# Optimization experiments

Hardware: AMD Instinct MI355X
Metric: run time of the kernel (lower is better)

The kernel has to match this reference:

```python
import jax, jax.numpy as jnp
import numpy as np

N_NODES = 50000
N_EDGES = 800000
D = 256          # in_features == out_features == num_classes
T = 4            # number of replicas / linear heads
NS = 64          # num_edges (hyperedges)


def setup_inputs() -> dict:
    key = jax.random.key(0)
    ks = jax.random.split(key, 10)
    s = D ** -0.5
    return {
        "edge_index": jax.random.randint(ks[0], (2, N_EDGES), 0, N_NODES, dtype=jnp.int64)
        if jax.config.jax_enable_x64 else jax.random.randint(ks[0], (2, N_EDGES), 0, N_NODES, dtype=jnp.int32),
        "features": jax.random.normal(ks[1], (N_NODES, D), jnp.float32),
        "lin_w": jax.random.normal(ks[2], (T, D, D), jnp.float32) * s,
        "lin_b": jax.random.normal(ks[3], (T, D), jnp.float32) * 0.01,
        "gcn0_w": jax.random.normal(ks[4], (D, D), jnp.float32) * s,
        "gcn0_b": jax.random.normal(ks[5], (D,), jnp.float32) * 0.01,
        "gcn1_w": jax.random.normal(ks[6], (D, D), jnp.float32) * s,
        "gcn1_b": jax.random.normal(ks[7], (D,), jnp.float32) * 0.01,
        "lin1_w": jax.random.normal(ks[8], (D, NS), jnp.float32) * s,
        "lin1_b": jax.random.normal(ks[9], (NS,), jnp.float32) * 0.01,
    }


def _l2_normalize(x, eps=1e-8):
    n = jnp.sqrt(jnp.sum(x * x, axis=-1, keepdims=True))
    return x / jnp.maximum(n, eps)


def reference(edge_index, features, lin_w, lin_b, gcn0_w, gcn0_b, gcn1_w, gcn1_b, lin1_w, lin1_b):
    num_nodes, d = features.shape
    t = lin_w.shape[0]
    ns = lin1_w.shape[1]
    scale = d ** -0.5  # out_features ** -0.5

    # t linear projections: (t, N, D)
    transformed = jnp.einsum('nd,tdk->tnk', features, lin_w) + lin_b[:, None, :]

    src, dst = edge_index[0], edge_index[1]
    # cosine similarity of features[src] vs each replica's transformed[dst]
    fs = _l2_normalize(features)[src]              # (E, D)
    tf_n = _l2_normalize(transformed)              # (t, N, D)
    sim = jnp.stack([jnp.sum(fs * tf_n[i][dst], axis=-1) for i in range(t)], axis=1)  # (E, t)
    best_idx = jnp.argmax(sim, axis=1)
    best_dst = dst + best_idx.astype(dst.dtype) * num_nodes

    # extra per-replica identity edges: node n -> node n + i*N, i in [0, t)
    ar = jnp.arange(num_nodes, dtype=src.dtype)
    extra_src = jnp.tile(ar, t)
    extra_dst = (ar[None, :] + (jnp.arange(t, dtype=src.dtype) * num_nodes)[:, None]).reshape(-1)

    src_all = jnp.concatenate([src, src, extra_src])
    dst_all = jnp.concatenate([dst, best_dst, extra_dst])
    n_total = (t + 1) * num_nodes

    # PyG gcn_norm: drop pre-existing self loops (weight 0), add one self loop per node,
    # symmetric normalization with degree from destination index.
    loops = jnp.arange(n_total, dtype=src.dtype)
    src2 = jnp.concatenate([src_all, loops])
    dst2 = jnp.concatenate([dst_all, loops])
    w2 = jnp.concatenate([jnp.where(src_all == dst_all, 0.0, 1.0).astype(features.dtype),
                          jnp.ones(n_total, features.dtype)])
    deg = jax.ops.segment_sum(w2, dst2, num_segments=n_total)
    dinv = jnp.where(deg > 0, jax.lax.rsqrt(deg), 0.0)
    norm = w2 * dinv[src2] * dinv[dst2]

    def gcn(x, W, b):
        xw = x @ W
        return jax.ops.segment_sum(norm[:, None] * xw[src2], dst2, num_segments=n_total) + b

    all_features = jnp.concatenate([features, transformed.reshape(t * num_nodes, d)], axis=0)
    # dropout is identity in eval mode
    h = jax.nn.relu(all_features)
    h = gcn(h, gcn0_w, gcn0_b)
    h = jax.nn.relu(h)
    all_features2 = gcn(h, gcn1_w, gcn1_b)          # ((t+1)N, D)
    logits = jax.nn.relu(all_features2) @ lin1_w + lin1_b  # ((t+1)N, NS)

    # H[n, c] counts how many of the (t+1) replicas assign node n to cluster c
    classes = jnp.argmax(logits.reshape(t + 1, num_nodes, ns), axis=-1)  # (t+1, N)
    H = jax.nn.one_hot(classes, ns, dtype=features.dtype).sum(axis=0)     # (N, NS)

    # hyperedge features: sum of all_features2 over base-replica nodes in each hyperedge
    mask = (H > 0).astype(features.dtype)                                  # (N, NS)
    hyperedge_features = mask.T @ all_features2[:num_nodes]                # (NS, D)

    dots = (all_features @ hyperedge_features.T) * scale                   # ((t+1)N, NS)
    return H, hyperedge_features, dots
```

## Files before the change

### kernel.cpp

```cpp
#include <hip/hip_runtime.h>

#define D 256
#define T 4
#define NS 64

typedef unsigned int uint32;
typedef short s16x8 __attribute__((ext_vector_type(8)));
typedef float f32x4 __attribute__((ext_vector_type(4)));

__device__ __forceinline__ float bflo(uint32 u) { return __uint_as_float(u << 16); }
__device__ __forceinline__ float bfhi(uint32 u) { return __uint_as_float(u & 0xffff0000u); }
__device__ __forceinline__ unsigned short f2bf(float x) {
    uint32 u = __float_as_uint(x);
    u = u + 0x7FFFu + ((u >> 16) & 1u);
    return (unsigned short)(u >> 16);
}
__device__ __forceinline__ uint32 pack2(float a, float b) {
    return (uint32)f2bf(a) | ((uint32)f2bf(b) << 16);
}
__device__ __forceinline__ uint32 relu2(uint32 u) {
    uint32 s = u & 0x80008000u;
    uint32 m = ((s >> 15) ^ 0x00010001u) * 0xFFFFu;
    return u & m;
}

__global__ void zero_kernel(uint32* __restrict__ p, long long n)
{
    long long i = (long long)blockIdx.x * blockDim.x + threadIdx.x;
    long long st = (long long)gridDim.x * blockDim.x;
    for (; i < n; i += st) p[i] = 0u;
}

__global__ void f2bf_kernel(const float* __restrict__ in, unsigned short* __restrict__ out,
                            long long n8)
{
    long long i = (long long)blockIdx.x * blockDim.x + threadIdx.x;
    long long st = (long long)gridDim.x * blockDim.x;
    for (; i < n8; i += st) {
        float4 a = *(const float4*)(in + i * 8);
        float4 b = *(const float4*)(in + i * 8 + 4);
        uint4 o;
        o.x = pack2(a.x, a.y); o.y = pack2(a.z, a.w);
        o.z = pack2(b.x, b.y); o.w = pack2(b.z, b.w);
        *(uint4*)(out + i * 8) = o;
    }
}

__global__ void wfrag_kernel(const float* __restrict__ g0, const float* __restrict__ g1,
                             const float* __restrict__ lw, unsigned short* __restrict__ out)
{
    int o = blockIdx.x * 256 + threadIdx.x;
    int mat = blockIdx.y;
    const float* W = (mat == 0) ? g0 : (mat == 1) ? g1 : (lw + (size_t)(mat - 2) * 65536);
    int j = o & 7, lane = (o >> 3) & 63, ks = (o >> 9) & 7, nt = o >> 12;
    int n15 = lane & 15, quad = lane >> 4;
    int k = ks * 32 + quad * 8 + j;
    int n = nt * 16 + n15;
    out[(size_t)mat * 65536 + o] = f2bf(W[(size_t)k * 256 + n]);
}

__global__ __launch_bounds__(256, 2)
void gemm_mfma(const unsigned short* __restrict__ A,
               const unsigned short* __restrict__ Wfrag,
               const float* __restrict__ bias,
               unsigned short* __restrict__ Cout,
               int M, int nStripes)
{
    __shared__ unsigned short Asm[64 * 264];
    int t = threadIdx.x, w = t >> 6, lane = t & 63;
    int n15 = lane & 15, quad = lane >> 4;
    int z = blockIdx.y;
    Wfrag += (size_t)z * 65536;
    bias  += (size_t)z * 256;
    Cout  += (size_t)z * (size_t)M * 256;

    s16x8 bfr[4][8];
#pragma unroll
    for (int nt = 0; nt < 4; nt++)
#pragma unroll
        for (int ks = 0; ks < 8; ks++)
            bfr[nt][ks] = *(const s16x8*)(Wfrag +
                (size_t)(((w * 4 + nt) * 8 + ks) * 64 + lane) * 8);

    float bcol[4];
#pragma unroll
    for (int nt = 0; nt < 4; nt++) bcol[nt] = bias[(w * 4 + nt) * 16 + n15];

    for (int s = blockIdx.x; s < nStripes; s += gridDim.x) {
        int m0 = s * 64;
        __syncthreads();
#pragma unroll
        for (int i = 0; i < 8; i++) {
            int idx = i * 256 + t;
            int m = idx >> 5, kc = (idx & 31) * 8;
            int gm = m0 + m;
            uint4 v = make_uint4(0u, 0u, 0u, 0u);
            if (gm < M) v = *(const uint4*)(A + (size_t)gm * 256 + kc);
            *(uint4*)(Asm + m * 264 + kc) = v;
        }
        __syncthreads();

        f32x4 acc[4][4];
#pragma unroll
        for (int rt = 0; rt < 4; rt++)
#pragma unroll
            for (int nt = 0; nt < 4; nt++)
#pragma unroll
                for (int e = 0; e < 4; e++) acc[rt][nt][e] = 0.f;

#pragma unroll
        for (int rt = 0; rt < 4; rt++) {
            int abase = (rt * 16 + n15) * 264 + quad * 8;
#pragma unroll
            for (int ks = 0; ks < 8; ks++) {
                s16x8 a = *(const s16x8*)(Asm + abase + ks * 32);
#pragma unroll
                for (int nt = 0; nt < 4; nt++)
                    acc[rt][nt] = __builtin_amdgcn_mfma_f32_16x16x32_bf16(
                        a, bfr[nt][ks], acc[rt][nt], 0, 0, 0);
            }
        }

#pragma unroll
        for (int rt = 0; rt < 4; rt++) {
            int row0 = m0 + rt * 16 + quad * 4;
#pragma unroll
            for (int nt = 0; nt < 4; nt++) {
                int colp = (w * 4 + nt) * 16 + n15;
#pragma unroll
                for (int r = 0; r < 4; r++) {
                    int gr = row0 + r;
                    if (gr < M)
                        Cout[(size_t)gr * 256 + colp] = f2bf(acc[rt][nt][r] + bcol[nt]);
                }
            }
        }
    }
}

__global__ __launch_bounds__(256)
void tinv_kernel(const unsigned short* __restrict__ tr, float* __restrict__ tinv, int rows)
{
    int wave = threadIdx.x >> 6, lane = threadIdx.x & 63;
    int r = blockIdx.x * 4 + wave;
    if (r >= rows) return;
    uint2 q = *(const uint2*)(tr + (size_t)r * D + lane * 4);
    float a = bflo(q.x), b = bfhi(q.x), c = bflo(q.y), d = bfhi(q.y);
    float s = a * a + b * b + c * c + d * d;
#pragma unroll
    for (int off = 32; off; off >>= 1) s += __shfl_xor(s, off);
    if (lane == 0) tinv[r] = 1.f / fmaxf(sqrtf(s), 1e-8f);
}

__global__ void ehist_kernel(const int* __restrict__ dst, int* __restrict__ ecnt, int E)
{
    for (int e = blockIdx.x * blockDim.x + threadIdx.x; e < E;
         e += gridDim.x * blockDim.x)
        atomicAdd(ecnt + dst[e], 1);
}

__global__ void escatter_kernel(const int* __restrict__ src, const int* __restrict__ dst,
                                const int* __restrict__ eptr, int* __restrict__ efill,
                                uint2* __restrict__ esorted, int E)
{
    for (int e = blockIdx.x * blockDim.x + threadIdx.x; e < E;
         e += gridDim.x * blockDim.x) {
        int d = dst[e];
        int pos = eptr[d] + atomicAdd(efill + d, 1);
        esorted[pos] = make_uint2((uint32)src[e], (uint32)d);
    }
}

__global__ __launch_bounds__(256)
void sim3_kernel(const uint2* __restrict__ esorted,
                 const unsigned short* __restrict__ featb,
                 const unsigned short* __restrict__ tr, const float* __restrict__ tinv,
                 int* __restrict__ bestS, int E, int Nn)
{
    int w = threadIdx.x >> 6, lane = threadIdx.x & 63;
    int n15 = lane & 15, quad = lane >> 4;
    int base = (blockIdx.x * 4 + w) * 16;
    if (base >= E) return;
    int ei = min(base + n15, E - 1);
    uint2 se = esorted[ei];
    const unsigned short* arow = featb + (size_t)se.x * D + quad * 8;
    const unsigned short* brow = tr + (size_t)se.y * D + quad * 8;
    size_t rstride = (size_t)Nn * D;

    f32x4 a0 = {0.f, 0.f, 0.f, 0.f}, a1 = a0, a2 = a0, a3 = a0;
#pragma unroll
    for (int ks = 0; ks < 8; ks++) {
        s16x8 a  = *(const s16x8*)(arow + ks * 32);
        s16x8 b0 = *(const s16x8*)(brow + ks * 32);
        s16x8 b1 = *(const s16x8*)(brow + rstride + ks * 32);
        s16x8 b2 = *(const s16x8*)(brow + 2 * rstride + ks * 32);
        s16x8 b3 = *(const s16x8*)(brow + 3 * rstride + ks * 32);
        a0 = __builtin_amdgcn_mfma_f32_16x16x32_bf16(a, b0, a0, 0, 0, 0);
        a1 = __builtin_amdgcn_mfma_f32_16x16x32_bf16(a, b1, a1, 0, 0, 0);
        a2 = __builtin_amdgcn_mfma_f32_16x16x32_bf16(a, b2, a2, 0, 0, 0);
        a3 = __builtin_amdgcn_mfma_f32_16x16x32_bf16(a, b3, a3, 0, 0, 0);
    }
    if (quad == (n15 >> 2) && base + n15 < E) {
        int r = n15 & 3;
        int d = (int)se.y;
        float v0 = a0[r] * tinv[d];
        float v1 = a1[r] * tinv[Nn + d];
        float v2 = a2[r] * tinv[2 * Nn + d];
        float v3 = a3[r] * tinv[3 * Nn + d];
        float bv = v0; int bi = 0;
        if (v1 > bv) { bv = v1; bi = 1; }
        if (v2 > bv) { bv = v2; bi = 2; }
        if (v3 > bv) { bv = v3; bi = 3; }
        bestS[base + n15] = bi;
    }
}

__device__ __forceinline__ void decode_edge(int e, const uint2* __restrict__ esorted,
                                            const int* __restrict__ bestS,
                                            int E, int Nn, int& s, int& d, bool& keep)
{
    if (e < E) {
        uint2 se = esorted[e];
        s = (int)se.x; d = (int)se.y; keep = (s != d);
    } else if (e < 2 * E) {
        int k = e - E;
        uint2 se = esorted[k];
        s = (int)se.x; d = (int)se.y + bestS[k] * Nn; keep = (s != d);
    } else if (e < 2 * E + T * Nn) {
        int k = e - 2 * E; int i = k / Nn; int n = k - i * Nn;
        s = n; d = n + i * Nn; keep = (i != 0);
    } else {
        int v = e - (2 * E + T * Nn); s = v; d = v; keep = true;
    }
}

__global__ void hist_kernel(const uint2* __restrict__ esorted, const int* __restrict__ bestS,
                            int* __restrict__ cnt, int E, int Nn)
{
    int total = 2 * E + (2 * T + 1) * Nn;
    for (int e = blockIdx.x * blockDim.x + threadIdx.x; e < total;
         e += gridDim.x * blockDim.x) {
        int s, d; bool keep;
        decode_edge(e, esorted, bestS, E, Nn, s, d, keep);
        if (keep) atomicAdd(cnt + d, 1);
    }
}

__global__ void dinv_kernel(const int* __restrict__ cnt, float* __restrict__ dinv, int n)
{
    int v = blockIdx.x * blockDim.x + threadIdx.x;
    if (v < n) dinv[v] = (cnt[v] > 0) ? rsqrtf((float)cnt[v]) : 0.f;
}

__global__ void emeta_kernel(const uint2* __restrict__ esorted, const int* __restrict__ bestS,
                             const float* __restrict__ dinv, uint2* __restrict__ emeta, int E)
{
    for (int e = blockIdx.x * blockDim.x + threadIdx.x; e < E;
         e += gridDim.x * blockDim.x) {
        uint2 se = esorted[e];
        uint32 packed = se.x | ((uint32)bestS[e] << 27);
        emeta[e] = make_uint2(packed, __float_as_uint(dinv[se.x]));
    }
}

__global__ void scan_sums(const int* __restrict__ cnt, int* __restrict__ aux, int n)
{
    __shared__ int sd[256];
    int idx = blockIdx.x * 256 + threadIdx.x;
    sd[threadIdx.x] = (idx < n) ? cnt[idx] : 0;
    __syncthreads();
    for (int off = 128; off; off >>= 1) {
        if (threadIdx.x < off) sd[threadIdx.x] += sd[threadIdx.x + off];
        __syncthreads();
    }
    if (threadIdx.x == 0) aux[blockIdx.x] = sd[0];
}

__global__ void scan_aux(const int* __restrict__ aux, int* __restrict__ auxex, int nb)
{
    __shared__ int sd[1024];
    int t = threadIdx.x;
    int v = (t < nb) ? aux[t] : 0;
    sd[t] = v;
    __syncthreads();
    for (int off = 1; off < 1024; off <<= 1) {
        int x = (t >= off) ? sd[t - off] : 0;
        __syncthreads();
        sd[t] += x;
        __syncthreads();
    }
    if (t < nb) auxex[t] = sd[t] - v;
}

__global__ void scan_write(const int* __restrict__ cnt, const int* __restrict__ auxex,
                           int* __restrict__ rowptr, int n)
{
    __shared__ int sd[256];
    int t = threadIdx.x;
    int idx = blockIdx.x * 256 + t;
    int v = (idx < n) ? cnt[idx] : 0;
    sd[t] = v;
    __syncthreads();
    for (int off = 1; off < 256; off <<= 1) {
        int x = (t >= off) ? sd[t - off] : 0;
        __syncthreads();
        sd[t] += x;
        __syncthreads();
    }
    if (idx < n) {
        int rp = auxex[blockIdx.x] + sd[t] - v;
        rowptr[idx] = rp;
        if (idx == n - 1) rowptr[n] = rp + v;
    }
}

__global__ __launch_bounds__(256)
void agg5_kernel(const int* __restrict__ eptr, const uint2* __restrict__ emeta,
                 const unsigned short* __restrict__ xa,
                 const unsigned short* __restrict__ xb,
                 const float* __restrict__ dinv,
                 unsigned short* __restrict__ outb, int Nn)
{
    int wave = threadIdx.x >> 6, lane = threadIdx.x & 63;
    int v = blockIdx.x * 4 + wave;
    if (v >= Nn) return;

    float dv  = dinv[v];
    float dr1 = dinv[v + Nn];
    float dr2 = dinv[v + 2 * Nn];
    float dr3 = dinv[v + 3 * Nn];
    float dr4 = dinv[v + 4 * Nn];

    uint2 qv = *(const uint2*)(xa + (size_t)v * D + lane * 4);
    qv.x = relu2(qv.x); qv.y = relu2(qv.y);
    float y0 = bflo(qv.x), y1 = bfhi(qv.x), y2 = bflo(qv.y), y3 = bfhi(qv.y);

    float wsb = dv * dv;
    float b0 = wsb * y0, b1 = wsb * y1, b2 = wsb * y2, b3 = wsb * y3;

    float wi1 = dv * dr1, wi2 = dv * dr2, wi3 = dv * dr3;
    float r10 = wi1 * y0, r11 = wi1 * y1, r12 = wi1 * y2, r13 = wi1 * y3;
    float r20 = wi2 * y0, r21 = wi2 * y1, r22 = wi2 * y2, r23 = wi2 * y3;
    float r30 = wi3 * y0, r31 = wi3 * y1, r32 = wi3 * y2, r33 = wi3 * y3;
    float r40 = 0.f, r41 = 0.f, r42 = 0.f, r43 = 0.f;

    {
        uint2 q = *(const uint2*)(xb + ((size_t)0 * Nn + v) * D + lane * 4);
        q.x = relu2(q.x); q.y = relu2(q.y);
        float ws = dr1 * dr1;
        r10 = fmaf(ws, bflo(q.x), r10); r11 = fmaf(ws, bfhi(q.x), r11);
        r12 = fmaf(ws, bflo(q.y), r12); r13 = fmaf(ws, bfhi(q.y), r13);
    }
    {
        uint2 q = *(const uint2*)(xb + ((size_t)1 * Nn + v) * D + lane * 4);
        q.x = relu2(q.x); q.y = relu2(q.y);
        float ws = dr2 * dr2;
        r20 = fmaf(ws, bflo(q.x), r20); r21 = fmaf(ws, bfhi(q.x), r21);
        r22 = fmaf(ws, bflo(q.y), r22); r23 = fmaf(ws, bfhi(q.y), r23);
    }
    {
        uint2 q = *(const uint2*)(xb + ((size_t)2 * Nn + v) * D + lane * 4);
        q.x = relu2(q.x); q.y = relu2(q.y);
        float ws = dr3 * dr3;
        r30 = fmaf(ws, bflo(q.x), r30); r31 = fmaf(ws, bfhi(q.x), r31);
        r32 = fmaf(ws, bflo(q.y), r32); r33 = fmaf(ws, bfhi(q.y), r33);
    }
    {
        uint2 q = *(const uint2*)(xb + ((size_t)3 * Nn + v) * D + lane * 4);
        q.x = relu2(q.x); q.y = relu2(q.y);
        float ws = dr4 * dr4;
        r40 = fmaf(ws, bflo(q.x), r40); r41 = fmaf(ws, bfhi(q.x), r41);
        r42 = fmaf(ws, bflo(q.y), r42); r43 = fmaf(ws, bfhi(q.y), r43);
    }

    int j = eptr[v], jend = eptr[v + 1];

#define EDGE_BODY(qq, ss, bb, ww)                                                  \
    {                                                                              \
        float x0 = bflo(qq.x), x1 = bfhi(qq.x), x2 = bflo(qq.y), x3 = bfhi(qq.y);  \
        float wb = (ss != v) ? (ww) * dv : 0.f;                                    \
        if (bb == 0) wb += wb;                                                     \
        b0 = fmaf(wb, x0, b0); b1 = fmaf(wb, x1, b1);                              \
        b2 = fmaf(wb, x2, b2); b3 = fmaf(wb, x3, b3);                              \
        if (bb == 1) {                                                             \
            float wr = (ww) * dr1;                                                 \
            r10 = fmaf(wr, x0, r10); r11 = fmaf(wr, x1, r11);                      \
            r12 = fmaf(wr, x2, r12); r13 = fmaf(wr, x3, r13);                      \
        } else if (bb == 2) {                                                      \
            float wr = (ww) * dr2;                                                 \
            r20 = fmaf(wr, x0, r20); r21 = fmaf(wr, x1, r21);                      \
            r22 = fmaf(wr, x2, r22); r23 = fmaf(wr, x3, r23);                      \
        } else if (bb == 3) {                                                      \
            float wr = (ww) * dr3;                                                 \
            r30 = fmaf(wr, x0, r30); r31 = fmaf(wr, x1, r31);                      \
            r32 = fmaf(wr, x2, r32); r33 = fmaf(wr, x3, r33);                      \
        }                                                                          \
    }

    for (; j + 2 <= jend; j += 2) {
        uint2 m0 = emeta[j];
        uint2 m1 = emeta[j + 1];
        uint32 su0 = (uint32)__builtin_amdgcn_readfirstlane((int)m0.x);
        uint32 su1 = (uint32)__builtin_amdgcn_readfirstlane((int)m1.x);
        float ws0 = __uint_as_float((uint32)__builtin_amdgcn_readfirstlane((int)m0.y));
        float ws1 = __uint_as_float((uint32)__builtin_amdgcn_readfirstlane((int)m1.y));
        int s0 = (int)(su0 & 0x07FFFFFFu), bx0 = (int)(su0 >> 27);
        int s1 = (int)(su1 & 0x07FFFFFFu), bx1 = (int)(su1 >> 27);
        uint2 q0 = *(const uint2*)(xa + (size_t)s0 * D + lane * 4);
        uint2 q1 = *(const uint2*)(xa + (size_t)s1 * D + lane * 4);
        q0.x = relu2(q0.x); q0.y = relu2(q0.y);
        q1.x = relu2(q1.x); q1.y = relu2(q1.y);
        EDGE_BODY(q0, s0, bx0, ws0);
        EDGE_BODY(q1, s1, bx1, ws1);
    }
    if (j < jend) {
        uint2 m0 = emeta[j];
        uint32 su0 = (uint32)__builtin_amdgcn_readfirstlane((int)m0.x);
        float ws0 = __uint_as_float((uint32)__builtin_amdgcn_readfirstlane((int)m0.y));
        int s0 = (int)(su0 & 0x07FFFFFFu), bx0 = (int)(su0 >> 27);
        uint2 q0 = *(const uint2*)(xa + (size_t)s0 * D + lane * 4);
        q0.x = relu2(q0.x); q0.y = relu2(q0.y);
        EDGE_BODY(q0, s0, bx0, ws0);
    }
#undef EDGE_BODY

    uint2 o;
    o.x = pack2(b0, b1); o.y = pack2(b2, b3);
    *(uint2*)(outb + (size_t)v * D + lane * 4) = o;
    o.x = pack2(r10, r11); o.y = pack2(r12, r13);
    *(uint2*)(outb + ((size_t)v + Nn) * D + lane * 4) = o;
    o.x = pack2(r20, r21); o.y = pack2(r22, r23);
    *(uint2*)(outb + ((size_t)v + 2 * (size_t)Nn) * D + lane * 4) = o;
    o.x = pack2(r30, r31); o.y = pack2(r32, r33);
    *(uint2*)(outb + ((size_t)v + 3 * (size_t)Nn) * D + lane * 4) = o;
    o.x = pack2(r40, r41); o.y = pack2(r42, r43);
    *(uint2*)(outb + ((size_t)v + 4 * (size_t)Nn) * D + lane * 4) = o;
}

__global__ __launch_bounds__(256, 2)
void logits_mfma(const unsigned short* __restrict__ af2, const float* __restrict__ Wl,
                 const float* __restrict__ bl, float* __restrict__ H,
                 int M, int Nn, int nStripes)
{
    __shared__ unsigned short Asm[64 * 264];
    int t = threadIdx.x, w = t >> 6, lane = t & 63;
    int n15 = lane & 15, quad = lane >> 4;

    s16x8 bfr[4][8];
#pragma unroll
    for (int nt = 0; nt < 4; nt++)
#pragma unroll
        for (int ks = 0; ks < 8; ks++) {
            s16x8 f;
#pragma unroll
            for (int j = 0; j < 8; j++) {
                int k = ks * 32 + quad * 8 + j;
                f[j] = (short)f2bf(Wl[(size_t)k * NS + nt * 16 + n15]);
            }
            bfr[nt][ks] = f;
        }
    float bcol[4];
#pragma unroll
    for (int nt = 0; nt < 4; nt++) bcol[nt] = bl[nt * 16 + n15];

    for (int s = blockIdx.x; s < nStripes; s += gridDim.x) {
        int m0 = s * 64;
        __syncthreads();
#pragma unroll
        for (int i = 0; i < 8; i++) {
            int idx = i * 256 + t;
            int m = idx >> 5, kc = (idx & 31) * 8;
            int gm = m0 + m;
            uint4 v = make_uint4(0u, 0u, 0u, 0u);
            if (gm < M) {
                v = *(const uint4*)(af2 + (size_t)gm * 256 + kc);
                v.x = relu2(v.x); v.y = relu2(v.y);
                v.z = relu2(v.z); v.w = relu2(v.w);
            }
            *(uint4*)(Asm + m * 264 + kc) = v;
        }
        __syncthreads();

        f32x4 acc[4];
#pragma unroll
        for (int nt = 0; nt < 4; nt++)
#pragma unroll
            for (int e = 0; e < 4; e++) acc[nt][e] = 0.f;

        int abase = (w * 16 + n15) * 264 + quad * 8;
#pragma unroll
        for (int ks = 0; ks < 8; ks++) {
            s16x8 a = *(const s16x8*)(Asm + abase + ks * 32);
#pragma unroll
            for (int nt = 0; nt < 4; nt++)
                acc[nt] = __builtin_amdgcn_mfma_f32_16x16x32_bf16(
                    a, bfr[nt][ks], acc[nt], 0, 0, 0);
        }

#pragma unroll
        for (int e = 0; e < 4; e++) {
            float bv = acc[0][e] + bcol[0]; int bi = n15;
#pragma unroll
            for (int nt = 1; nt < 4; nt++) {
                float v = acc[nt][e] + bcol[nt];
                int c = nt * 16 + n15;
                if (v > bv) { bv = v; bi = c; }
            }
#pragma unroll
            for (int off = 1; off < 16; off <<= 1) {
                float ov = __shfl_xor(bv, off);
                int   oi = __shfl_xor(bi, off);
                if (ov > bv || (ov == bv && oi < bi)) { bv = ov; bi = oi; }
            }
            if (n15 == 0) {
                int gr = m0 + w * 16 + quad * 4 + e;
                if (gr < M) atomicAdd(H + (size_t)(gr % Nn) * NS + bi, 1.0f);
            }
        }
    }
}

__global__ __launch_bounds__(64)
void he_kernel(const float* __restrict__ H, const unsigned short* __restrict__ af2,
               float* __restrict__ he, int Nn)
{
    __shared__ float acc[NS * D];
    int lane = threadIdx.x;
    for (int i = lane * 4; i < NS * D; i += 256)
        *(float4*)(acc + i) = make_float4(0.f, 0.f, 0.f, 0.f);
    __syncthreads();
    int n0 = blockIdx.x * 128;
    int n1 = min(n0 + 128, Nn);
    for (int n = n0; n < n1; n++) {
        float hv = H[(size_t)n * NS + lane];
        unsigned long long m = __ballot(hv > 0.f);
        if (!m) continue;
        uint2 q = *(const uint2*)(af2 + (size_t)n * D + lane * 4);
        float x0 = bflo(q.x), x1 = bfhi(q.x), x2 = bflo(q.y), x3 = bfhi(q.y);
        while (m) {
            int c = __ffsll(m) - 1;
            m &= m - 1;
            float* p = acc + (size_t)c * D + lane * 4;
            p[0] += x0; p[1] += x1; p[2] += x2; p[3] += x3;
        }
    }
    __syncthreads();
    for (int i = lane; i < NS * D; i += 64) atomicAdd(he + i, acc[i]);
}

__global__ void bigb_copy(const float* __restrict__ he, float* __restrict__ BigB)
{
    int idx = blockIdx.x * 256 + threadIdx.x;
    if (idx < D * NS) {
        int d = idx >> 6, c = idx & 63;
        BigB[idx] = he[(size_t)c * D + d];
    }
}

__global__ __launch_bounds__(256)
void bigb_mm(const float* __restrict__ lin_w, const float* __restrict__ lin_b,
             const float* __restrict__ he, float* __restrict__ BigB,
             float* __restrict__ beta)
{
    int gw = (int)((blockIdx.x * 256 + threadIdx.x) >> 6);
    int lane = threadIdx.x & 63;
    const int totalA = T * D * NS;
    if (gw >= totalA + T * NS) return;
    const float* xrow; const float* hrow; float* outp;
    if (gw < totalA) {
        int t = gw / (D * NS); int rem = gw - t * D * NS;
        int d = rem / NS; int c = rem - d * NS;
        xrow = lin_w + ((size_t)t * D + d) * D;
        hrow = he + (size_t)c * D;
        outp = BigB + ((size_t)(t + 1) * D + d) * NS + c;
    } else {
        int i = gw - totalA; int t = i / NS; int c = i - t * NS;
        xrow = lin_b + (size_t)t * D;
        hrow = he + (size_t)c * D;
        outp = beta + (size_t)(t + 1) * NS + c;
    }
    float4 x = *(const float4*)(xrow + lane * 4);
    float4 h = *(const float4*)(hrow + lane * 4);
    float s = x.x * h.x + x.y * h.y + x.z * h.z + x.w * h.w;
#pragma unroll
    for (int off = 32; off; off >>= 1) s += __shfl_xor(s, off);
    if (lane == 0) *outp = s;
}

__global__ __launch_bounds__(256, 2)
void dots_mfma(const float* __restrict__ feat, const float* __restrict__ BigB,
               const float* __restrict__ beta, float* __restrict__ dots,
               int Nn, int nStripes)
{
    __shared__ unsigned short Asm[64 * 264];
    int t = threadIdx.x, w = t >> 6, lane = t & 63;
    int n15 = lane & 15, quad = lane >> 4;
    int rho = blockIdx.y;
    const float* Bp = BigB + (size_t)rho * D * NS;

    s16x8 bfr[4][8];
#pragma unroll
    for (int nt = 0; nt < 4; nt++)
#pragma unroll
        for (int ks = 0; ks < 8; ks++) {
            s16x8 f;
#pragma unroll
            for (int j = 0; j < 8; j++) {
                int k = ks * 32 + quad * 8 + j;
                f[j] = (short)f2bf(Bp[(size_t)k * NS + nt * 16 + n15]);
            }
            bfr[nt][ks] = f;
        }
    float bcol[4];
#pragma unroll
    for (int nt = 0; nt < 4; nt++) bcol[nt] = beta[rho * NS + nt * 16 + n15];

    for (int s = blockIdx.x; s < nStripes; s += gridDim.x) {
        int m0 = s * 64;
        __syncthreads();
#pragma unroll
        for (int i = 0; i < 8; i++) {
            int idx = i * 256 + t;
            int m = idx >> 5, kc = (idx & 31) * 8;
            int gm = m0 + m;
            uint4 o = make_uint4(0u, 0u, 0u, 0u);
            if (gm < Nn) {
                float4 a = *(const float4*)(feat + (size_t)gm * 256 + kc);
                float4 b = *(const float4*)(feat + (size_t)gm * 256 + kc + 4);
                o.x = pack2(a.x, a.y); o.y = pack2(a.z, a.w);
                o.z = pack2(b.x, b.y); o.w = pack2(b.z, b.w);
            }
            *(uint4*)(Asm + m * 264 + kc) = o;
        }
        __syncthreads();

        f32x4 acc[4];
#pragma unroll
        for (int nt = 0; nt < 4; nt++)
#pragma unroll
            for (int e = 0; e < 4; e++) acc[nt][e] = 0.f;

        int abase = (w * 16 + n15) * 264 + quad * 8;
#pragma unroll
        for (int ks = 0; ks < 8; ks++) {
            s16x8 a = *(const s16x8*)(Asm + abase + ks * 32);
#pragma unroll
            for (int nt = 0; nt < 4; nt++)
                acc[nt] = __builtin_amdgcn_mfma_f32_16x16x32_bf16(
                    a, bfr[nt][ks], acc[nt], 0, 0, 0);
        }

#pragma unroll
        for (int e = 0; e < 4; e++) {
            int gr = m0 + w * 16 + quad * 4 + e;
            if (gr >= Nn) continue;
#pragma unroll
            for (int nt = 0; nt < 4; nt++) {
                int c = nt * 16 + n15;
                dots[((size_t)rho * Nn + gr) * NS + c] = (acc[nt][e] + bcol[nt]) * 0.0625f;
            }
        }
    }
}

extern "C" void kernel_launch(void* const* d_in, const int* in_sizes, int n_in,
                              void* d_out, int out_size, void* d_ws, size_t ws_size,
                              hipStream_t stream)
{
    const int*   edge_index = (const int*)d_in[0];
    const float* features   = (const float*)d_in[1];
    const float* lin_w      = (const float*)d_in[2];
    const float* lin_b      = (const float*)d_in[3];
    const float* gcn0_w     = (const float*)d_in[4];
    const float* gcn0_b     = (const float*)d_in[5];
    const float* gcn1_w     = (const float*)d_in[6];
    const float* gcn1_b     = (const float*)d_in[7];
    const float* lin1_w     = (const float*)d_in[8];
    const float* lin1_b     = (const float*)d_in[9];

    int E  = in_sizes[0] / 2;
    int Nn = in_sizes[1] / D;
    int n_total = (T + 1) * Nn;
    int Mrep = T * Nn;

    const int* src = edge_index;
    const int* dst = edge_index + E;

    float* out_H    = (float*)d_out;
    float* out_he   = out_H + (size_t)Nn * NS;
    float* out_dots = out_he + (size_t)NS * D;

    char* ws = (char*)d_ws;
    auto carve = [&](size_t bytes) {
        char* p = ws; ws += (bytes + 255) & ~(size_t)255; return p;
    };
    unsigned short* R1   = (unsigned short*)carve((size_t)n_total * D * 2);
    unsigned short* R2   = (unsigned short*)carve((size_t)n_total * D * 2);
    float*          BigB = (float*)carve((size_t)(T + 1) * D * NS * 4);
    float*          beta = (float*)carve((size_t)(T + 1) * NS * 4);
    unsigned short* transformed = R2;

    char* sc = (char*)out_dots;
    auto carve2 = [&](size_t bytes) {
        char* p = sc; sc += (bytes + 255) & ~(size_t)255; return p;
    };
    float* tinv    = (float*)carve2((size_t)Mrep * 4);
    int*   best    = (int*)carve2((size_t)E * 4);
    int*   cnt     = (int*)carve2((size_t)n_total * 4);
    float* dinv    = (float*)carve2((size_t)n_total * 4);
    int*   aux     = (int*)carve2(1024 * 4);
    int*   auxex   = (int*)carve2(1024 * 4);
    unsigned short* featb  = (unsigned short*)carve2((size_t)Nn * D * 2);
    unsigned short* Wfrags = (unsigned short*)carve2((size_t)6 * 65536 * 2);
    int*   ecnt    = (int*)carve2((size_t)Nn * 4);
    int*   eptr    = (int*)carve2((size_t)(Nn + 1) * 4);
    int*   efill   = (int*)carve2((size_t)Nn * 4);
    uint2* esorted = (uint2*)carve2((size_t)E * 8);
    uint2* emeta   = (uint2*)carve2((size_t)E * 8);

    zero_kernel<<<512, 256, 0, stream>>>((uint32*)cnt, n_total);
    zero_kernel<<<512, 256, 0, stream>>>((uint32*)ecnt, Nn);
    zero_kernel<<<512, 256, 0, stream>>>((uint32*)efill, Nn);
    zero_kernel<<<512, 256, 0, stream>>>((uint32*)out_H, (long long)Nn * NS + NS * D);
    zero_kernel<<<1, 256, 0, stream>>>((uint32*)beta, (T + 1) * NS);

    wfrag_kernel<<<dim3(256, 6), 256, 0, stream>>>(gcn0_w, gcn1_w, lin_w, Wfrags);
    f2bf_kernel<<<2048, 256, 0, stream>>>(features, featb, (long long)Nn * D / 8);

    int strN = (Nn + 63) / 64;
    gemm_mfma<<<dim3(512, T), 256, 0, stream>>>(featb, Wfrags + 2 * 65536, lin_b,
                                                transformed, Nn, strN);
    tinv_kernel<<<(Mrep + 3) / 4, 256, 0, stream>>>(transformed, tinv, Mrep);

    ehist_kernel<<<2048, 256, 0, stream>>>(dst, ecnt, E);
    int enb = (Nn + 255) / 256;
    scan_sums<<<enb, 256, 0, stream>>>(ecnt, aux, Nn);
    scan_aux<<<1, 1024, 0, stream>>>(aux, auxex, enb);
    scan_write<<<enb, 256, 0, stream>>>(ecnt, auxex, eptr, Nn);
    escatter_kernel<<<2048, 256, 0, stream>>>(src, dst, eptr, efill, esorted, E);
    int nGroups = (E + 15) / 16;
    sim3_kernel<<<(nGroups + 3) / 4, 256, 0, stream>>>(esorted, featb, transformed,
                                                       tinv, best, E, Nn);

    hist_kernel<<<2048, 256, 0, stream>>>(esorted, best, cnt, E, Nn);
    dinv_kernel<<<(n_total + 255) / 256, 256, 0, stream>>>(cnt, dinv, n_total);
    emeta_kernel<<<2048, 256, 0, stream>>>(esorted, best, dinv, emeta, E);

    int strT = (n_total + 63) / 64;
    agg5_kernel<<<(Nn + 3) / 4, 256, 0, stream>>>(eptr, emeta, featb, transformed,
                                                  dinv, R1, Nn);
    gemm_mfma<<<dim3(512, 1), 256, 0, stream>>>(R1, Wfrags, gcn0_b, R1, n_total, strT);

    agg5_kernel<<<(Nn + 3) / 4, 256, 0, stream>>>(eptr, emeta, R1, R1 + (size_t)Nn * D,
                                                  dinv, R2, Nn);
    gemm_mfma<<<dim3(512, 1), 256, 0, stream>>>(R2, Wfrags + 65536, gcn1_b, R2,
                                                n_total, strT);

    logits_mfma<<<512, 256, 0, stream>>>(R2, lin1_w, lin1_b, out_H, n_total, Nn, strT);

    he_kernel<<<(Nn + 127) / 128, 64, 0, stream>>>(out_H, R2, out_he, Nn);

    bigb_copy<<<(D * NS + 255) / 256, 256, 0, stream>>>(out_he, BigB);
    bigb_mm<<<(T * D * NS + T * NS + 3) / 4, 256, 0, stream>>>(lin_w, lin_b, out_he,
                                                               BigB, beta);
    dots_mfma<<<dim3(160, 5), 256, 0, stream>>>(features, BigB, beta, out_dots,
                                                Nn, strN);
}
```

Measured before the change: 1.072 ms.

## Restructure hyperedge sum via transposed mask and reuse bf16 features in dots

The old hyperedge kernel walked nodes serially per block and accumulated into a 64KB shared buffer, then flushed it with many global atomics. It is replaced by a kernel that writes a transposed byte mask of H, followed by a per-(cluster, node-chunk) warp reduction that gathers the selected af2 rows in registers and issues one atomic per element. Separately, the bf16 feature copy is placed in workspace when space allows so the dots kernel can read bf16 directly instead of converting fp32 again. Work is now proportional to nonzero mask entries, with one gather per entry rather than a shared-memory update, and there is an extra kernel launch plus mask memory traffic.

```diff
diff --git a/kernel.cpp b/kernel.cpp
--- a/kernel.cpp
+++ b/kernel.cpp
@@ -520,32 +520,72 @@
     }
 }
 
-__global__ __launch_bounds__(64)
-void he_kernel(const float* __restrict__ H, const unsigned short* __restrict__ af2,
-               float* __restrict__ he, int Nn)
-{
-    __shared__ float acc[NS * D];
-    int lane = threadIdx.x;
-    for (int i = lane * 4; i < NS * D; i += 256)
-        *(float4*)(acc + i) = make_float4(0.f, 0.f, 0.f, 0.f);
+__global__ __launch_bounds__(256)
+void maskT_kernel(const float* __restrict__ H, unsigned char* __restrict__ maskT, int Nn)
+{
+    __shared__ unsigned char tile[64 * 80];
+    int t = threadIdx.x;
+    int n0 = blockIdx.x * 64;
+    int c = t & 63, rr = t >> 6;
+#pragma unroll
+    for (int i = 0; i < 16; i++) {
+        int n = rr + i * 4;
+        float hv = (n0 + n < Nn) ? H[(size_t)(n0 + n) * NS + c] : 0.f;
+        tile[c * 80 + n] = (hv > 0.f) ? 1 : 0;
+    }
     __syncthreads();
-    int n0 = blockIdx.x * 128;
-    int n1 = min(n0 + 128, Nn);
-    for (int n = n0; n < n1; n++) {
-        float hv = H[(size_t)n * NS + lane];
-        unsigned long long m = __ballot(hv > 0.f);
-        if (!m) continue;
-        uint2 q = *(const uint2*)(af2 + (size_t)n * D + lane * 4);
-        float x0 = bflo(q.x), x1 = bfhi(q.x), x2 = bflo(q.y), x3 = bfhi(q.y);
-        while (m) {
-            int c = __ffsll(m) - 1;
-            m &= m - 1;
-            float* p = acc + (size_t)c * D + lane * 4;
-            p[0] += x0; p[1] += x1; p[2] += x2; p[3] += x3;
-        }
-    }
-    __syncthreads();
-    for (int i = lane; i < NS * D; i += 64) atomicAdd(he + i, acc[i]);
+    int cc = t >> 2, ns = (t & 3) * 16;
+    if (n0 + ns < Nn) {
+        uint4 v = *(const uint4*)(tile + cc * 80 + ns);
+        *(uint4*)(maskT + (size_t)cc * Nn + n0 + ns) = v;
+    }
+}
+
+#define HE_NSPLIT 64
+__global__ __launch_bounds__(256)
+void he2_kernel(const unsigned char* __restrict__ maskT,
+                const unsigned short* __restrict__ af2,
+                float* __restrict__ he, int Nn, int chunk)
+{
+    int w = threadIdx.x >> 6, lane = threadIdx.x & 63;
+    int gw = blockIdx.x * 4 + w;
+    int c = gw / HE_NSPLIT;
+    int s = gw - c * HE_NSPLIT;
+    int n0 = s * chunk;
+    int n1 = min(n0 + chunk, Nn);
+    if (n0 >= n1) return;
+    const unsigned char* mrow = maskT + (size_t)c * Nn;
+    float a0 = 0.f, a1 = 0.f, a2 = 0.f, a3 = 0.f;
+
+    for (int nb = n0; nb < n1; nb += 256) {
+        uint32 mb = 0;
+        if (n1 - nb >= 256) {
+            mb = *(const uint32*)(mrow + nb + lane * 4);
+        } else {
+#pragma unroll
+            for (int k = 0; k < 4; k++) {
+                int n = nb + lane * 4 + k;
+                if (n < n1) mb |= ((uint32)mrow[n]) << (8 * k);
+            }
+        }
+#pragma unroll
+        for (int k = 0; k < 4; k++) {
+            unsigned long long m = __ballot(((mb >> (8 * k)) & 0xffu) != 0u);
+            while (m) {
+                int l = __ffsll(m) - 1;
+                m &= m - 1;
+                int n = nb + l * 4 + k;
+                uint2 q = *(const uint2*)(af2 + (size_t)n * D + lane * 4);
+                a0 += bflo(q.x); a1 += bfhi(q.x);
+                a2 += bflo(q.y); a3 += bfhi(q.y);
+            }
+        }
+    }
+    float* p = he + (size_t)c * D + lane * 4;
+    atomicAdd(p + 0, a0);
+    atomicAdd(p + 1, a1);
+    atomicAdd(p + 2, a2);
+    atomicAdd(p + 3, a3);
 }
 
 __global__ void bigb_copy(const float* __restrict__ he, float* __restrict__ BigB)
@@ -588,7 +628,9 @@
 }
 
 __global__ __launch_bounds__(256, 2)
-void dots_mfma(const float* __restrict__ feat, const float* __restrict__ BigB,
+void dots_mfma(const unsigned short* __restrict__ featb,
+               const float* __restrict__ feat32, int useBf,
+               const float* __restrict__ BigB,
                const float* __restrict__ beta, float* __restrict__ dots,
                int Nn, int nStripes)
 {
@@ -625,10 +667,14 @@
             int gm = m0 + m;
             uint4 o = make_uint4(0u, 0u, 0u, 0u);
             if (gm < Nn) {
-                float4 a = *(const float4*)(feat + (size_t)gm * 256 + kc);
-                float4 b = *(const float4*)(feat + (size_t)gm * 256 + kc + 4);
-                o.x = pack2(a.x, a.y); o.y = pack2(a.z, a.w);
-                o.z = pack2(b.x, b.y); o.w = pack2(b.z, b.w);
+                if (useBf) {
+                    o = *(const uint4*)(featb + (size_t)gm * 256 + kc);
+                } else {
+                    float4 a = *(const float4*)(feat32 + (size_t)gm * 256 + kc);
+                    float4 b = *(const float4*)(feat32 + (size_t)gm * 256 + kc + 4);
+                    o.x = pack2(a.x, a.y); o.y = pack2(a.z, a.w);
+                    o.z = pack2(b.x, b.y); o.w = pack2(b.z, b.w);
+                }
             }
             *(uint4*)(Asm + m * 264 + kc) = o;
         }
@@ -690,15 +736,24 @@
     float* out_he   = out_H + (size_t)Nn * NS;
     float* out_dots = out_he + (size_t)NS * D;
 
-    char* ws = (char*)d_ws;
+    char* ws0 = (char*)d_ws;
+    char* wsp = ws0;
     auto carve = [&](size_t bytes) {
-        char* p = ws; ws += (bytes + 255) & ~(size_t)255; return p;
+        char* p = wsp; wsp += (bytes + 255) & ~(size_t)255; return p;
     };
     unsigned short* R1   = (unsigned short*)carve((size_t)n_total * D * 2);
     unsigned short* R2   = (unsigned short*)carve((size_t)n_total * D * 2);
     float*          BigB = (float*)carve((size_t)(T + 1) * D * NS * 4);
     float*          beta = (float*)carve((size_t)(T + 1) * NS * 4);
     unsigned short* transformed = R2;
+
+    size_t featb_bytes = (size_t)Nn * D * 2;
+    unsigned short* featb = nullptr;
+    int useBfDots = 0;
+    if ((size_t)(wsp - ws0) + featb_bytes + 256 <= ws_size) {
+        featb = (unsigned short*)carve(featb_bytes);
+        useBfDots = 1;
+    }
 
     char* sc = (char*)out_dots;
     auto carve2 = [&](size_t bytes) {
@@ -710,13 +765,14 @@
     float* dinv    = (float*)carve2((size_t)n_total * 4);
     int*   aux     = (int*)carve2(1024 * 4);
     int*   auxex   = (int*)carve2(1024 * 4);
-    unsigned short* featb  = (unsigned short*)carve2((size_t)Nn * D * 2);
+    if (!featb) featb = (unsigned short*)carve2(featb_bytes);
     unsigned short* Wfrags = (unsigned short*)carve2((size_t)6 * 65536 * 2);
     int*   ecnt    = (int*)carve2((size_t)Nn * 4);
     int*   eptr    = (int*)carve2((size_t)(Nn + 1) * 4);
     int*   efill   = (int*)carve2((size_t)Nn * 4);
     uint2* esorted = (uint2*)carve2((size_t)E * 8);
     uint2* emeta   = (uint2*)carve2((size_t)E * 8);
+    unsigned char* maskT = (unsigned char*)carve2((size_t)NS * Nn);
 
     zero_kernel<<<512, 256, 0, stream>>>((uint32*)cnt, n_total);
     zero_kernel<<<512, 256, 0, stream>>>((uint32*)ecnt, Nn);
@@ -758,11 +814,13 @@
 
     logits_mfma<<<512, 256, 0, stream>>>(R2, lin1_w, lin1_b, out_H, n_total, Nn, strT);
 
-    he_kernel<<<(Nn + 127) / 128, 64, 0, stream>>>(out_H, R2, out_he, Nn);
+    maskT_kernel<<<(Nn + 63) / 64, 256, 0, stream>>>(out_H, maskT, Nn);
+    int chunk = (Nn + HE_NSPLIT - 1) / HE_NSPLIT;
+    he2_kernel<<<(NS * HE_NSPLIT) / 4, 256, 0, stream>>>(maskT, R2, out_he, Nn, chunk);
 
     bigb_copy<<<(D * NS + 255) / 256, 256, 0, stream>>>(out_he, BigB);
     bigb_mm<<<(T * D * NS + T * NS + 3) / 4, 256, 0, stream>>>(lin_w, lin_b, out_he,
                                                                BigB, beta);
-    dots_mfma<<<dim3(160, 5), 256, 0, stream>>>(features, BigB, beta, out_dots,
-                                                Nn, strN);
-}
+    dots_mfma<<<dim3(160, 5), 256, 0, stream>>>(featb, features, useBfDots,
+                                                BigB, beta, out_dots, Nn, strN);
+}
```

New measurement: 1.164 ms. 8.5% more time.

## Reuse bf16 features in dots kernel and parallelize hyperedge accumulation

Applied to the files above, without the earlier changes.

Moves the bf16 feature copy into workspace when space allows, so the dots kernel reads half-width features instead of converting fp32 for every replica pass. The hyperedge kernel is restructured into 256-thread blocks that split the feature dimension in two halves, with four waves sharing a smaller LDS accumulator via LDS atomics and software-prefetching the next row. The goal is to reduce global read traffic and raise occupancy, at the cost of LDS atomic contention and a workspace-size dependent path.

```diff
diff --git a/kernel.cpp b/kernel.cpp
--- a/kernel.cpp
+++ b/kernel.cpp
@@ -520,32 +520,49 @@
     }
 }
 
-__global__ __launch_bounds__(64)
-void he_kernel(const float* __restrict__ H, const unsigned short* __restrict__ af2,
-               float* __restrict__ he, int Nn)
-{
-    __shared__ float acc[NS * D];
-    int lane = threadIdx.x;
-    for (int i = lane * 4; i < NS * D; i += 256)
+__global__ __launch_bounds__(256)
+void he3_kernel(const float* __restrict__ H, const unsigned short* __restrict__ af2,
+                float* __restrict__ he, int Nn)
+{
+    __shared__ float acc[NS * 128];
+    int t = threadIdx.x, w = t >> 6, lane = t & 63;
+    int half = blockIdx.y;
+
+    for (int i = t * 4; i < NS * 128; i += 1024)
         *(float4*)(acc + i) = make_float4(0.f, 0.f, 0.f, 0.f);
     __syncthreads();
-    int n0 = blockIdx.x * 128;
+
+    int n0 = blockIdx.x * 512 + w * 128;
     int n1 = min(n0 + 128, Nn);
-    for (int n = n0; n < n1; n++) {
-        float hv = H[(size_t)n * NS + lane];
-        unsigned long long m = __ballot(hv > 0.f);
-        if (!m) continue;
-        uint2 q = *(const uint2*)(af2 + (size_t)n * D + lane * 4);
-        float x0 = bflo(q.x), x1 = bfhi(q.x), x2 = bflo(q.y), x3 = bfhi(q.y);
-        while (m) {
-            int c = __ffsll(m) - 1;
-            m &= m - 1;
-            float* p = acc + (size_t)c * D + lane * 4;
-            p[0] += x0; p[1] += x1; p[2] += x2; p[3] += x3;
+    const unsigned short* xbase = af2 + half * 128 + lane * 2;
+
+    if (n0 < n1) {
+        float hv = H[(size_t)n0 * NS + lane];
+        uint32 xr = *(const uint32*)(xbase + (size_t)n0 * D);
+        for (int n = n0; n < n1; n++) {
+            float chv = hv;
+            uint32 cx = xr;
+            if (n + 1 < n1) {
+                hv = H[(size_t)(n + 1) * NS + lane];
+                xr = *(const uint32*)(xbase + (size_t)(n + 1) * D);
+            }
+            unsigned long long m = __ballot(chv > 0.f);
+            float x0 = bflo(cx), x1 = bfhi(cx);
+            while (m) {
+                int c = __ffsll(m) - 1;
+                m &= m - 1;
+                float* p = acc + c * 128 + lane * 2;
+                atomicAdd(p, x0);
+                atomicAdd(p + 1, x1);
+            }
         }
     }
     __syncthreads();
-    for (int i = lane; i < NS * D; i += 64) atomicAdd(he + i, acc[i]);
+
+    for (int i = t; i < NS * 128; i += 256) {
+        int c = i >> 7, f = i & 127;
+        atomicAdd(he + (size_t)c * D + half * 128 + f, acc[i]);
+    }
 }
 
 __global__ void bigb_copy(const float* __restrict__ he, float* __restrict__ BigB)
@@ -588,7 +605,9 @@
 }
 
 __global__ __launch_bounds__(256, 2)
-void dots_mfma(const float* __restrict__ feat, const float* __restrict__ BigB,
+void dots_mfma(const unsigned short* __restrict__ featb,
+               const float* __restrict__ feat32, int useBf,
+               const float* __restrict__ BigB,
                const float* __restrict__ beta, float* __restrict__ dots,
                int Nn, int nStripes)
 {
@@ -625,10 +644,14 @@
             int gm = m0 + m;
             uint4 o = make_uint4(0u, 0u, 0u, 0u);
             if (gm < Nn) {
-                float4 a = *(const float4*)(feat + (size_t)gm * 256 + kc);
-                float4 b = *(const float4*)(feat + (size_t)gm * 256 + kc + 4);
-                o.x = pack2(a.x, a.y); o.y = pack2(a.z, a.w);
-                o.z = pack2(b.x, b.y); o.w = pack2(b.z, b.w);
+                if (useBf) {
+                    o = *(const uint4*)(featb + (size_t)gm * 256 + kc);
+                } else {
+                    float4 a = *(const float4*)(feat32 + (size_t)gm * 256 + kc);
+                    float4 b = *(const float4*)(feat32 + (size_t)gm * 256 + kc + 4);
+                    o.x = pack2(a.x, a.y); o.y = pack2(a.z, a.w);
+                    o.z = pack2(b.x, b.y); o.w = pack2(b.z, b.w);
+                }
             }
             *(uint4*)(Asm + m * 264 + kc) = o;
         }
@@ -690,15 +713,24 @@
     float* out_he   = out_H + (size_t)Nn * NS;
     float* out_dots = out_he + (size_t)NS * D;
 
-    char* ws = (char*)d_ws;
+    char* ws0 = (char*)d_ws;
+    char* wsp = ws0;
     auto carve = [&](size_t bytes) {
-        char* p = ws; ws += (bytes + 255) & ~(size_t)255; return p;
+        char* p = wsp; wsp += (bytes + 255) & ~(size_t)255; return p;
     };
     unsigned short* R1   = (unsigned short*)carve((size_t)n_total * D * 2);
     unsigned short* R2   = (unsigned short*)carve((size_t)n_total * D * 2);
     float*          BigB = (float*)carve((size_t)(T + 1) * D * NS * 4);
     float*          beta = (float*)carve((size_t)(T + 1) * NS * 4);
     unsigned short* transformed = R2;
+
+    size_t featb_bytes = (size_t)Nn * D * 2;
+    unsigned short* featb = nullptr;
+    int useBfDots = 0;
+    if ((size_t)(wsp - ws0) + featb_bytes + 256 <= ws_size) {
+        featb = (unsigned short*)carve(featb_bytes);
+        useBfDots = 1;
+    }
 
     char* sc = (char*)out_dots;
     auto carve2 = [&](size_t bytes) {
@@ -710,7 +742,7 @@
     float* dinv    = (float*)carve2((size_t)n_total * 4);
     int*   aux     = (int*)carve2(1024 * 4);
     int*   auxex   = (int*)carve2(1024 * 4);
-    unsigned short* featb  = (unsigned short*)carve2((size_t)Nn * D * 2);
+    if (!featb) featb = (unsigned short*)carve2(featb_bytes);
     unsigned short* Wfrags = (unsigned short*)carve2((size_t)6 * 65536 * 2);
     int*   ecnt    = (int*)carve2((size_t)Nn * 4);
     int*   eptr    = (int*)carve2((size_t)(Nn + 1) * 4);
@@ -758,11 +790,11 @@
 
     logits_mfma<<<512, 256, 0, stream>>>(R2, lin1_w, lin1_b, out_H, n_total, Nn, strT);
 
-    he_kernel<<<(Nn + 127) / 128, 64, 0, stream>>>(out_H, R2, out_he, Nn);
+    he3_kernel<<<dim3((Nn + 511) / 512, 2), 256, 0, stream>>>(out_H, R2, out_he, Nn);
 
     bigb_copy<<<(D * NS + 255) / 256, 256, 0, stream>>>(out_he, BigB);
     bigb_mm<<<(T * D * NS + T * NS + 3) / 4, 256, 0, stream>>>(lin_w, lin_b, out_he,
                                                                BigB, beta);
-    dots_mfma<<<dim3(160, 5), 256, 0, stream>>>(features, BigB, beta, out_dots,
-                                                Nn, strN);
-}
+    dots_mfma<<<dim3(160, 5), 256, 0, stream>>>(featb, features, useBfDots,
+                                                BigB, beta, out_dots, Nn, strN);
+}
```

Result: no change. 1.072 ms (-0.0%).
